# Optimization experiments

Measured on AMD Instinct MI355X. Metric: run time of the kernel, lower is better.

The kernel has to match this reference:

```python
import jax, jax.numpy as jnp
import numpy as np

N_CODES = 8192
EMBED_DIM = 64
N_VOXELS = 32768


def setup_inputs() -> dict:
    key = jax.random.key(0)
    k1, k2 = jax.random.split(key)
    z_feats = jax.random.normal(k1, (N_VOXELS, EMBED_DIM), dtype=jnp.float32)
    embeddings = jax.random.normal(k2, (N_CODES, EMBED_DIM), dtype=jnp.float32)
    return {"z_feats": z_feats, "embeddings": embeddings}


def reference(z_feats, embeddings):
    # Pairwise squared euclidean distances: ||z||^2 - 2 z.e + ||e||^2  [N, K]
    z_sq = jnp.sum(z_feats * z_feats, axis=1, keepdims=True)        # [N, 1]
    e_sq = jnp.sum(embeddings * embeddings, axis=1)[None, :]        # [1, K]
    d2 = z_sq - 2.0 * jnp.einsum('nd,kd->nk', z_feats, embeddings) + e_sq
    # argmin is invariant under sqrt (cdist returns sqrt, but only indices are used)
    encoding_indices = jnp.argmin(d2, axis=1)                        # [N]
    quantized_feats = embeddings[encoding_indices]                   # [N, D]
    # commitment_loss = mse(z, sg(q));  vq_loss = mse(q, sg(z)) (gradient mode)
    commitment_loss = jnp.mean((z_feats - jax.lax.stop_gradient(quantized_feats)) ** 2)
    vq_loss = jnp.mean((quantized_feats - jax.lax.stop_gradient(z_feats)) ** 2)
    # straight-through estimator
    quantized_st = z_feats + jax.lax.stop_gradient(quantized_feats - z_feats)
    indices_out = encoding_indices[:, None].astype(jnp.float32)      # [N, 1]
    return quantized_st, vq_loss, commitment_loss, indices_out
```

## Files before the change

### kernel.cpp

```cpp
#include <hip/hip_runtime.h>
#include <float.h>

#define N_VOX 32768
#define N_CODES 8192
#define DIM 64

#define Q_OFF 0
#define VQ_OFF (N_VOX * DIM)
#define CM_OFF (VQ_OFF + 1)
#define IDX_OFF (VQ_OFF + 2)

#define WS_ACC 0
#define WS_CNT 1
#define WS_ESQH 64
#define WS_EHI (WS_ESQH + N_CODES)
#define WS_ELO (WS_EHI + N_CODES * DIM / 2)

typedef _Float16 half8 __attribute__((ext_vector_type(8)));
typedef float floatx4 __attribute__((ext_vector_type(4)));

__global__ __launch_bounds__(256) void k_cvt(const float* __restrict__ e,
                                             float* __restrict__ ws) {
  int gid = blockIdx.x * 256 + threadIdx.x;
  if (gid == 0) { ws[WS_ACC] = 0.f; ((int*)ws)[WS_CNT] = 0; }
  int row = gid >> 3, c = gid & 7;
  const float* src = e + (size_t)row * DIM + c * 8;
  float4 a = *(const float4*)src;
  float4 b = *(const float4*)(src + 4);
  float x[8] = {a.x, a.y, a.z, a.w, b.x, b.y, b.z, b.w};
  float s = 0.f;
  half8 hv, lv;
  #pragma unroll
  for (int j = 0; j < 8; ++j) {
    s += x[j] * x[j];
    _Float16 h = (_Float16)x[j];
    hv[j] = h;
    lv[j] = (_Float16)(x[j] - (float)h);
  }
  s += __shfl_xor(s, 1); s += __shfl_xor(s, 2); s += __shfl_xor(s, 4);
  if (c == 0) ws[WS_ESQH + row] = 0.5f * s;
  int g = row >> 4, n = row & 15, kc = c >> 2, q = c & 3;
  size_t p = (size_t)g * 128 + kc * 64 + n * 4 + q;
  ((half8*)(ws + WS_EHI))[p] = hv;
  ((half8*)(ws + WS_ELO))[p] = lv;
}

__global__ __launch_bounds__(256, 2) void k_argmin(const float* __restrict__ z,
                                                   const float* __restrict__ e,
                                                   float* __restrict__ ws,
                                                   float* __restrict__ out) {
  __shared__ float sMval[4][64];
  __shared__ int   sMidx[4][64];
  __shared__ float sZsq[64];
  __shared__ int   sIdxF[64];

  const int tid  = threadIdx.x;
  const int lane = tid & 63;
  const int wave = tid >> 6;
  const int n16  = lane & 15;
  const int quad = lane >> 4;
  const int vb   = blockIdx.x * 64;
  const int wbase = wave * 2048;

  half8 ahi[4][2], alo[4][2];
  float zsq[4] = {0.f, 0.f, 0.f, 0.f};
  #pragma unroll
  for (int m = 0; m < 4; ++m)
    #pragma unroll
    for (int kc = 0; kc < 2; ++kc) {
      const float* src = z + (size_t)(vb + m * 16 + n16) * DIM + kc * 32 + quad * 8;
      float4 a = *(const float4*)src;
      float4 b = *(const float4*)(src + 4);
      float x[8] = {a.x, a.y, a.z, a.w, b.x, b.y, b.z, b.w};
      #pragma unroll
      for (int j = 0; j < 8; ++j) {
        zsq[m] += x[j] * x[j];
        _Float16 h = (_Float16)x[j];
        ahi[m][kc][j] = h;
        alo[m][kc][j] = (_Float16)(x[j] - (float)h);
      }
    }
  #pragma unroll
  for (int m = 0; m < 4; ++m) {
    zsq[m] += __shfl_xor(zsq[m], 16);
    zsq[m] += __shfl_xor(zsq[m], 32);
  }
  if (wave == 0 && quad == 0)
    #pragma unroll
    for (int m = 0; m < 4; ++m) sZsq[m * 16 + n16] = zsq[m];

  float bval[4][4]; int bidx[4][4];
  #pragma unroll
  for (int m = 0; m < 4; ++m)
    #pragma unroll
    for (int r = 0; r < 4; ++r) { bval[m][r] = FLT_MAX; bidx[m][r] = 0; }

  const half8* __restrict__ bhp = (const half8*)(ws + WS_EHI);
  const half8* __restrict__ blp = (const half8*)(ws + WS_ELO);
  const float* __restrict__ esq = ws + WS_ESQH;
  const size_t rbase = (size_t)wave * 16384 + n16 * 4 + quad;

  auto step = [&](half8 b0, half8 b1, half8 b2, half8 b3, float e2, int codebase) {
    floatx4 acc[4];
    #pragma unroll
    for (int m = 0; m < 4; ++m) acc[m] = (floatx4){0.f, 0.f, 0.f, 0.f};
    #pragma unroll
    for (int m = 0; m < 4; ++m) acc[m] = __builtin_amdgcn_mfma_f32_16x16x32_f16(ahi[m][0], b0, acc[m], 0, 0, 0);
    #pragma unroll
    for (int m = 0; m < 4; ++m) acc[m] = __builtin_amdgcn_mfma_f32_16x16x32_f16(ahi[m][1], b1, acc[m], 0, 0, 0);
    #pragma unroll
    for (int m = 0; m < 4; ++m) acc[m] = __builtin_amdgcn_mfma_f32_16x16x32_f16(ahi[m][0], b2, acc[m], 0, 0, 0);
    #pragma unroll
    for (int m = 0; m < 4; ++m) acc[m] = __builtin_amdgcn_mfma_f32_16x16x32_f16(ahi[m][1], b3, acc[m], 0, 0, 0);
    #pragma unroll
    for (int m = 0; m < 4; ++m) acc[m] = __builtin_amdgcn_mfma_f32_16x16x32_f16(alo[m][0], b0, acc[m], 0, 0, 0);
    #pragma unroll
    for (int m = 0; m < 4; ++m) acc[m] = __builtin_amdgcn_mfma_f32_16x16x32_f16(alo[m][1], b1, acc[m], 0, 0, 0);
    const int code = codebase + n16;
    #pragma unroll
    for (int m = 0; m < 4; ++m)
      #pragma unroll
      for (int r = 0; r < 4; ++r) {
        float tv = e2 - acc[m][r];
        if (tv < bval[m][r]) { bval[m][r] = tv; bidx[m][r] = code; }
      }
  };

  half8 pa0 = bhp[rbase], pa1 = bhp[rbase + 64];
  half8 pa2 = blp[rbase], pa3 = blp[rbase + 64];
  float pae = esq[wbase + n16];
  half8 pb0, pb1, pb2, pb3; float pbe;

  for (int g = 0; g < 128; g += 2) {
    {
      size_t rb = rbase + (size_t)(g + 1) * 128;
      pb0 = bhp[rb];  pb1 = bhp[rb + 64];
      pb2 = blp[rb];  pb3 = blp[rb + 64];
      pbe = esq[wbase + (g + 1) * 16 + n16];
    }
    step(pa0, pa1, pa2, pa3, pae, wbase + g * 16);
    if (g + 2 < 128) {
      size_t rb = rbase + (size_t)(g + 2) * 128;
      pa0 = bhp[rb];  pa1 = bhp[rb + 64];
      pa2 = blp[rb];  pa3 = blp[rb + 64];
      pae = esq[wbase + (g + 2) * 16 + n16];
    }
    step(pb0, pb1, pb2, pb3, pbe, wbase + (g + 1) * 16);
  }

  #pragma unroll
  for (int m = 0; m < 4; ++m)
    #pragma unroll
    for (int r = 0; r < 4; ++r) {
      float v = bval[m][r]; int i = bidx[m][r];
      #pragma unroll
      for (int off = 1; off < 16; off <<= 1) {
        float ov = __shfl_xor(v, off);
        int   oi = __shfl_xor(i, off);
        if (ov < v || (ov == v && oi < i)) { v = ov; i = oi; }
      }
      if (n16 == 0) {
        int vox = m * 16 + quad * 4 + r;
        sMval[wave][vox] = v; sMidx[wave][vox] = i;
      }
    }
  __syncthreads();

  if (tid < 64) {
    float best = sMval[0][tid]; int bi = sMidx[0][tid];
    #pragma unroll
    for (int w = 1; w < 4; ++w) {
      float ov = sMval[w][tid]; int oi = sMidx[w][tid];
      if (ov < best || (ov == best && oi < bi)) { best = ov; bi = oi; }
    }
    out[IDX_OFF + vb + tid] = (float)bi;
    sIdxF[tid] = bi;
    float d2 = sZsq[tid] + 2.0f * best;
    #pragma unroll
    for (int off = 1; off < 64; off <<= 1) d2 += __shfl_xor(d2, off);
    if (tid == 0) atomicAdd(ws + WS_ACC, d2);
  }
  __syncthreads();

  for (int i = tid; i < 1024; i += 256) {
    int v = i >> 4, c = i & 15;
    int idx = sIdxF[v];
    float4 q = *(const float4*)(e + (size_t)idx * DIM + c * 4);
    *(float4*)(out + Q_OFF + (size_t)(vb + v) * DIM + c * 4) = q;
  }

  __threadfence();
  if (tid == 0) {
    int old = atomicAdd((int*)ws + WS_CNT, 1);
    if (old == (int)gridDim.x - 1) {
      __threadfence();
      float s = atomicAdd(ws + WS_ACC, 0.0f);
      float m = s * (1.0f / (float)(N_VOX * DIM));
      out[VQ_OFF] = m;
      out[CM_OFF] = m;
    }
  }
}

extern "C" void kernel_launch(void* const* d_in, const int* in_sizes, int n_in,
                              void* d_out, int out_size, void* d_ws, size_t ws_size,
                              hipStream_t stream) {
  const float* z = (const float*)d_in[0];
  const float* e = (const float*)d_in[1];
  float* out = (float*)d_out;
  float* ws = (float*)d_ws;

  k_cvt<<<(N_CODES * 8) / 256, 256, 0, stream>>>(e, ws);
  k_argmin<<<N_VOX / 64, 256, 0, stream>>>(z, e, ws, out);
}
```

Baseline: 210.1 us.

## Split codebook search across four blocks per tile and add merge kernel

Each 64-voxel tile is now processed by four blocks, each scanning a quarter of the codebook and writing its best value and index to workspace. A new merge kernel picks the minimum per voxel, gathers the code row, writes outputs and computes the loss directly from z minus the selected code. This shortens per-block work and raises grid size for better balance, at the cost of an extra launch, partial-result traffic and redundant A-fragment conversion per slice.

```diff
diff --git a/kernel.cpp b/kernel.cpp
--- a/kernel.cpp
+++ b/kernel.cpp
@@ -15,6 +15,7 @@
 #define WS_ESQH 64
 #define WS_EHI (WS_ESQH + N_CODES)
 #define WS_ELO (WS_EHI + N_CODES * DIM / 2)
+#define WS_PART (WS_ELO + N_CODES * DIM / 2)
 
 typedef _Float16 half8 __attribute__((ext_vector_type(8)));
 typedef float floatx4 __attribute__((ext_vector_type(4)));
@@ -46,24 +47,20 @@
 }
 
 __global__ __launch_bounds__(256, 2) void k_argmin(const float* __restrict__ z,
-                                                   const float* __restrict__ e,
-                                                   float* __restrict__ ws,
-                                                   float* __restrict__ out) {
+                                                   float* __restrict__ ws) {
   __shared__ float sMval[4][64];
   __shared__ int   sMidx[4][64];
-  __shared__ float sZsq[64];
-  __shared__ int   sIdxF[64];
 
   const int tid  = threadIdx.x;
   const int lane = tid & 63;
   const int wave = tid >> 6;
   const int n16  = lane & 15;
   const int quad = lane >> 4;
-  const int vb   = blockIdx.x * 64;
-  const int wbase = wave * 2048;
+  const int vb    = (blockIdx.x >> 2) * 64;
+  const int slice = blockIdx.x & 3;
+  const int gbase = slice * 128 + wave * 32;
 
   half8 ahi[4][2], alo[4][2];
-  float zsq[4] = {0.f, 0.f, 0.f, 0.f};
   #pragma unroll
   for (int m = 0; m < 4; ++m)
     #pragma unroll
@@ -74,20 +71,11 @@
       float x[8] = {a.x, a.y, a.z, a.w, b.x, b.y, b.z, b.w};
       #pragma unroll
       for (int j = 0; j < 8; ++j) {
-        zsq[m] += x[j] * x[j];
         _Float16 h = (_Float16)x[j];
         ahi[m][kc][j] = h;
         alo[m][kc][j] = (_Float16)(x[j] - (float)h);
       }
     }
-  #pragma unroll
-  for (int m = 0; m < 4; ++m) {
-    zsq[m] += __shfl_xor(zsq[m], 16);
-    zsq[m] += __shfl_xor(zsq[m], 32);
-  }
-  if (wave == 0 && quad == 0)
-    #pragma unroll
-    for (int m = 0; m < 4; ++m) sZsq[m * 16 + n16] = zsq[m];
 
   float bval[4][4]; int bidx[4][4];
   #pragma unroll
@@ -98,7 +86,7 @@
   const half8* __restrict__ bhp = (const half8*)(ws + WS_EHI);
   const half8* __restrict__ blp = (const half8*)(ws + WS_ELO);
   const float* __restrict__ esq = ws + WS_ESQH;
-  const size_t rbase = (size_t)wave * 16384 + n16 * 4 + quad;
+  const size_t rbase = (size_t)gbase * 128 + n16 * 4 + quad;
 
   auto step = [&](half8 b0, half8 b1, half8 b2, half8 b3, float e2, int codebase) {
     floatx4 acc[4];
@@ -128,24 +116,24 @@
 
   half8 pa0 = bhp[rbase], pa1 = bhp[rbase + 64];
   half8 pa2 = blp[rbase], pa3 = blp[rbase + 64];
-  float pae = esq[wbase + n16];
+  float pae = esq[gbase * 16 + n16];
   half8 pb0, pb1, pb2, pb3; float pbe;
 
-  for (int g = 0; g < 128; g += 2) {
+  for (int g = 0; g < 32; g += 2) {
     {
       size_t rb = rbase + (size_t)(g + 1) * 128;
       pb0 = bhp[rb];  pb1 = bhp[rb + 64];
       pb2 = blp[rb];  pb3 = blp[rb + 64];
-      pbe = esq[wbase + (g + 1) * 16 + n16];
-    }
-    step(pa0, pa1, pa2, pa3, pae, wbase + g * 16);
-    if (g + 2 < 128) {
+      pbe = esq[(gbase + g + 1) * 16 + n16];
+    }
+    step(pa0, pa1, pa2, pa3, pae, (gbase + g) * 16);
+    if (g + 2 < 32) {
       size_t rb = rbase + (size_t)(g + 2) * 128;
       pa0 = bhp[rb];  pa1 = bhp[rb + 64];
       pa2 = blp[rb];  pa3 = blp[rb + 64];
-      pae = esq[wbase + (g + 2) * 16 + n16];
-    }
-    step(pb0, pb1, pb2, pb3, pbe, wbase + (g + 1) * 16);
+      pae = esq[(gbase + g + 2) * 16 + n16];
+    }
+    step(pb0, pb1, pb2, pb3, pbe, (gbase + g + 1) * 16);
   }
 
   #pragma unroll
@@ -173,24 +161,48 @@
       float ov = sMval[w][tid]; int oi = sMidx[w][tid];
       if (ov < best || (ov == best && oi < bi)) { best = ov; bi = oi; }
     }
-    out[IDX_OFF + vb + tid] = (float)bi;
-    sIdxF[tid] = bi;
-    float d2 = sZsq[tid] + 2.0f * best;
-    #pragma unroll
-    for (int off = 1; off < 64; off <<= 1) d2 += __shfl_xor(d2, off);
-    if (tid == 0) atomicAdd(ws + WS_ACC, d2);
-  }
+    float2 p; p.x = best; p.y = __int_as_float(bi);
+    ((float2*)(ws + WS_PART))[(size_t)(vb + tid) * 4 + slice] = p;
+  }
+}
+
+__global__ __launch_bounds__(256) void k_merge(const float* __restrict__ z,
+                                               const float* __restrict__ e,
+                                               float* __restrict__ ws,
+                                               float* __restrict__ out) {
+  const int tid = threadIdx.x;
+  const int gid = blockIdx.x * 256 + tid;
+  const int vox = gid >> 4;
+  const int l4  = gid & 15;
+  const float2* __restrict__ part = (const float2*)(ws + WS_PART);
+
+  int bi = 0;
+  if (l4 == 0) {
+    float2 p0 = part[(size_t)vox * 4 + 0];
+    float best = p0.x; bi = __float_as_int(p0.y);
+    #pragma unroll
+    for (int s = 1; s < 4; ++s) {
+      float2 p = part[(size_t)vox * 4 + s];
+      if (p.x < best) { best = p.x; bi = __float_as_int(p.y); }
+    }
+    out[IDX_OFF + vox] = (float)bi;
+  }
+  bi = __shfl(bi, 0, 16);
+
+  float4 e4 = *(const float4*)(e + (size_t)bi * DIM + l4 * 4);
+  float4 z4 = *(const float4*)(z + (size_t)vox * DIM + l4 * 4);
+  *(float4*)(out + Q_OFF + (size_t)vox * DIM + l4 * 4) = e4;
+  float dx = z4.x - e4.x, dy = z4.y - e4.y, dz = z4.z - e4.z, dw = z4.w - e4.w;
+  float local = dx * dx + dy * dy + dz * dz + dw * dw;
+
+  #pragma unroll
+  for (int off = 32; off; off >>= 1) local += __shfl_xor(local, off);
+  __shared__ float wsum[4];
+  if ((tid & 63) == 0) wsum[tid >> 6] = local;
   __syncthreads();
-
-  for (int i = tid; i < 1024; i += 256) {
-    int v = i >> 4, c = i & 15;
-    int idx = sIdxF[v];
-    float4 q = *(const float4*)(e + (size_t)idx * DIM + c * 4);
-    *(float4*)(out + Q_OFF + (size_t)(vb + v) * DIM + c * 4) = q;
-  }
-
-  __threadfence();
   if (tid == 0) {
+    atomicAdd(ws + WS_ACC, wsum[0] + wsum[1] + wsum[2] + wsum[3]);
+    __threadfence();
     int old = atomicAdd((int*)ws + WS_CNT, 1);
     if (old == (int)gridDim.x - 1) {
       __threadfence();
@@ -211,5 +223,6 @@
   float* ws = (float*)d_ws;
 
   k_cvt<<<(N_CODES * 8) / 256, 256, 0, stream>>>(e, ws);
-  k_argmin<<<N_VOX / 64, 256, 0, stream>>>(z, e, ws, out);
-}
+  k_argmin<<<(N_VOX / 64) * 4, 256, 0, stream>>>(z, ws);
+  k_merge<<<(N_VOX * 16) / 256, 256, 0, stream>>>(z, e, ws, out);
+}
```

New measurement: 238.0 us. 13.3% more time.
